# Performance work log

Measured on AMD Instinct MI355X. Metric: run time of the kernel, lower is better.

## Reference

```python
import jax, jax.numpy as jnp
import numpy as np

ALPHA, GAMMA, EPS = 0.25, 2.0, 1e-8
COST_CLASS, COST_BBOX, COST_GIOU = 2.0, 5.0, 2.0


def box_cxcywh_to_xyxy(b):
    cx, cy, w, h = jnp.split(b, 4, axis=-1)
    return jnp.concatenate([cx - 0.5 * w, cy - 0.5 * h, cx + 0.5 * w, cy + 0.5 * h], axis=-1)


def setup_inputs() -> dict:
    key = jax.random.key(0)
    k1, k2, k3, k4 = jax.random.split(key, 4)
    bs, Q, C, T = 16, 900, 80, 1600
    return {
        "pred_logits": jax.random.normal(k1, (bs, Q, C), jnp.float32),
        "pred_boxes": jax.random.uniform(k2, (bs, Q, 4), jnp.float32),
        "tgt_labels": jax.random.randint(k3, (T,), 0, C),
        "tgt_boxes": jax.random.uniform(k4, (T, 4), jnp.float32),
        "g_size": 3,
    }


def reference(pred_logits, pred_boxes, tgt_labels, tgt_boxes, g_size):
    bs, Q, _ = pred_logits.shape
    # focal classification cost (use_focal=True path)
    p = jax.nn.sigmoid(pred_logits.reshape(bs * Q, -1))  # [N, C]
    neg = (1.0 - ALPHA) * p ** GAMMA * (-jnp.log(1.0 - p + EPS))
    pos = ALPHA * (1.0 - p) ** GAMMA * (-jnp.log(p + EPS))
    cost_class = (pos - neg)[:, tgt_labels]  # [N, T]
    # L1 box cost (cdist p=1)
    out_bbox = pred_boxes.reshape(bs * Q, 4)
    cost_bbox = jnp.abs(out_bbox[:, None, :] - tgt_bbox_b(tgt_boxes)).sum(-1)  # [N, T]
    # GIoU cost
    b1 = box_cxcywh_to_xyxy(out_bbox)  # [N, 4]
    b2 = box_cxcywh_to_xyxy(tgt_boxes)  # [T, 4]
    area1 = (b1[:, 2] - b1[:, 0]) * (b1[:, 3] - b1[:, 1])
    area2 = (b2[:, 2] - b2[:, 0]) * (b2[:, 3] - b2[:, 1])
    lt = jnp.maximum(b1[:, None, :2], b2[None, :, :2])
    rb = jnp.minimum(b1[:, None, 2:], b2[None, :, 2:])
    wh = jnp.clip(rb - lt, 0.0)
    inter = wh[..., 0] * wh[..., 1]
    union = area1[:, None] + area2[None, :] - inter
    iou = inter / union
    elt = jnp.minimum(b1[:, None, :2], b2[None, :, :2])
    erb = jnp.maximum(b1[:, None, 2:], b2[None, :, 2:])
    ewh = jnp.clip(erb - elt, 0.0)
    earea = ewh[..., 0] * ewh[..., 1]
    giou = iou - (earea - union) / earea
    # weighted total cost, then group reduction (note: original names it Cmin but takes max over the group dim)
    Cmat = COST_BBOX * cost_bbox + COST_CLASS * cost_class + COST_GIOU * (-giou)
    Cmin = Cmat.reshape(bs, Q // g_size, g_size, -1).max(axis=2)  # [bs, Q//g, T]
    return Cmin


def tgt_bbox_b(tgt_boxes):
    return tgt_boxes[None, :, :]
```

## Files before the change

### kernel.cpp

```cpp
#include <hip/hip_runtime.h>

#define ALPHA 0.25f
#define EPS   1e-8f

constexpr int BS    = 16;
constexpr int QN    = 900;
constexpr int CN    = 80;
constexpr int GS    = 3;
constexpr int WAVES = 4;
constexpr int NT    = WAVES * 64;
constexpr int ROWS  = WAVES * GS;
constexpr int CCPAD = 16;

__global__ __launch_bounds__(NT) void fused_cost_kernel(
    const float* __restrict__ pred_logits,
    const float* __restrict__ pred_boxes,
    const int*   __restrict__ tgt_labels,
    const float* __restrict__ tgt_boxes,
    float*       __restrict__ out,
    int T)
{
    __shared__ __align__(16) float s_cc[CN * CCPAD];

    const int tid  = threadIdx.x;
    const int wv   = tid >> 6;
    const int lane = tid & 63;
    const int b    = blockIdx.y;
    const int n0   = b * QN + blockIdx.x * ROWS;

    const float* lg0 = pred_logits + (size_t)n0 * CN;
    for (int k = tid; k < ROWS * CN; k += NT) {
        const int r = k / CN, c = k - r * CN;
        float x = lg0[k];
        float p = __fdividef(1.0f, 1.0f + __expf(-x));
        float omp = 1.0f - p;
        float pos = ALPHA * omp * omp * (-__logf(p + EPS));
        float neg = (1.0f - ALPHA) * p * p * (-__logf(omp + EPS));
        s_cc[c * CCPAD + r + r / GS] = pos - neg;
    }

    float Pcx[GS], Pcy[GS], Pw[GS], Ph[GS];
    float Px0[GS], Py0[GS], Px1[GS], Py1[GS], Pa[GS];
    #pragma unroll
    for (int g = 0; g < GS; ++g) {
        const float4 pb = ((const float4*)pred_boxes)[n0 + wv * GS + g];
        Pcx[g] = pb.x;  Pcy[g] = pb.y;  Pw[g] = pb.z;  Ph[g] = pb.w;
        Px0[g] = pb.x - 0.5f * pb.z;  Py0[g] = pb.y - 0.5f * pb.w;
        Px1[g] = pb.x + 0.5f * pb.z;  Py1[g] = pb.y + 0.5f * pb.w;
        Pa[g]  = pb.z * pb.w;
    }
    __syncthreads();

    const int qg = blockIdx.x * WAVES + wv;
    float* __restrict__ outp = out + (size_t)(b * (QN / GS) + qg) * T;
    const int ccBase = wv * 4;

    for (int t = lane; t < T; t += 64) {
        const float4 tr = ((const float4*)tgt_boxes)[t];
        const int lab   = tgt_labels[t];
        const float tx0 = tr.x - 0.5f * tr.z, ty0 = tr.y - 0.5f * tr.w;
        const float tx1 = tr.x + 0.5f * tr.z, ty1 = tr.y + 0.5f * tr.w;
        const float ta  = tr.z * tr.w;

        const float4 cc4 = *(const float4*)&s_cc[lab * CCPAD + ccBase];
        const float ccv[GS] = { cc4.x, cc4.y, cc4.z };

        float m = -3.402823466e+38f;
        #pragma unroll
        for (int g = 0; g < GS; ++g) {
            float l1 = fabsf(Pcx[g] - tr.x) + fabsf(Pcy[g] - tr.y)
                     + fabsf(Pw[g]  - tr.z) + fabsf(Ph[g]  - tr.w);

            float iw = fminf(Px1[g], tx1) - fmaxf(Px0[g], tx0);
            float ih = fminf(Py1[g], ty1) - fmaxf(Py0[g], ty0);
            float inter = fmaxf(iw, 0.0f) * fmaxf(ih, 0.0f);
            float uni   = Pa[g] + ta - inter;

            float ew = fmaxf(Px1[g], tx1) - fminf(Px0[g], tx0);
            float eh = fmaxf(Py1[g], ty1) - fminf(Py0[g], ty0);
            float earea = ew * eh;

            float num = fmaf(inter, earea, uni * uni);
            float den = uni * earea;
            float g2  = 2.0f * __fdividef(num, den);

            float cost = fmaf(5.0f, l1, fmaf(2.0f, ccv[g], 2.0f - g2));
            m = fmaxf(m, cost);
        }
        outp[t] = m;
    }
}

extern "C" void kernel_launch(void* const* d_in, const int* in_sizes, int n_in,
                              void* d_out, int out_size, void* d_ws, size_t ws_size,
                              hipStream_t stream) {
    const float* pred_logits = (const float*)d_in[0];
    const float* pred_boxes  = (const float*)d_in[1];
    const int*   tgt_labels  = (const int*)d_in[2];
    const float* tgt_boxes   = (const float*)d_in[3];

    const int T = in_sizes[2];
    float* out = (float*)d_out;

    dim3 grid((QN / GS) / WAVES, BS);
    fused_cost_kernel<<<grid, NT, 0, stream>>>(
        pred_logits, pred_boxes, tgt_labels, tgt_boxes, out, T);
}
```

Before: 104.9 us.

## Split target dimension across blocks and simplify class-cost smem layout

Adds a grid dimension that splits the T targets into two halves per block, doubling the block count while each block recomputes the 12-row focal-cost table. The smem table becomes row-major with the constant offset and the factor of 2 folded in, replacing one float4 LDS with three scalar reads. The target loop is unrolled by two with an explicit tail. The cost is redundant sigmoid/log work, since each logit block is now computed twice. It also assumes T divides evenly by TSPLIT.

```diff
diff --git a/kernel.cpp b/kernel.cpp
--- a/kernel.cpp
+++ b/kernel.cpp
@@ -3,14 +3,14 @@
 #define ALPHA 0.25f
 #define EPS   1e-8f
 
-constexpr int BS    = 16;
-constexpr int QN    = 900;
-constexpr int CN    = 80;
-constexpr int GS    = 3;
-constexpr int WAVES = 4;
-constexpr int NT    = WAVES * 64;
-constexpr int ROWS  = WAVES * GS;
-constexpr int CCPAD = 16;
+constexpr int BS     = 16;
+constexpr int QN     = 900;
+constexpr int CN     = 80;
+constexpr int GS     = 3;
+constexpr int WAVES  = 4;
+constexpr int NT     = WAVES * 64;
+constexpr int ROWS   = WAVES * GS;
+constexpr int TSPLIT = 2;
 
 __global__ __launch_bounds__(NT) void fused_cost_kernel(
     const float* __restrict__ pred_logits,
@@ -20,23 +20,23 @@
     float*       __restrict__ out,
     int T)
 {
-    __shared__ __align__(16) float s_cc[CN * CCPAD];
+    __shared__ float s_cc[ROWS * CN];
 
     const int tid  = threadIdx.x;
     const int wv   = tid >> 6;
     const int lane = tid & 63;
-    const int b    = blockIdx.y;
-    const int n0   = b * QN + blockIdx.x * ROWS;
+    const int b    = blockIdx.z;
+    const int n0   = b * QN + blockIdx.y * ROWS;
 
     const float* lg0 = pred_logits + (size_t)n0 * CN;
+    #pragma unroll
     for (int k = tid; k < ROWS * CN; k += NT) {
-        const int r = k / CN, c = k - r * CN;
         float x = lg0[k];
         float p = __fdividef(1.0f, 1.0f + __expf(-x));
         float omp = 1.0f - p;
         float pos = ALPHA * omp * omp * (-__logf(p + EPS));
         float neg = (1.0f - ALPHA) * p * p * (-__logf(omp + EPS));
-        s_cc[c * CCPAD + r + r / GS] = pos - neg;
+        s_cc[k] = 2.0f * (pos - neg) + 2.0f;
     }
 
     float Pcx[GS], Pcy[GS], Pw[GS], Ph[GS];
@@ -51,19 +51,25 @@
     }
     __syncthreads();
 
-    const int qg = blockIdx.x * WAVES + wv;
+    const int qg = blockIdx.y * WAVES + wv;
     float* __restrict__ outp = out + (size_t)(b * (QN / GS) + qg) * T;
-    const int ccBase = wv * 4;
+    const int ccRow = (wv * GS) * CN;
 
-    for (int t = lane; t < T; t += 64) {
+    const int tChunk = T / TSPLIT;
+    const int t0     = blockIdx.x * tChunk;
+    const int nFull  = tChunk >> 6;
+    const int tail   = tChunk & 63;
+
+    auto body = [&](int t) {
         const float4 tr = ((const float4*)tgt_boxes)[t];
         const int lab   = tgt_labels[t];
         const float tx0 = tr.x - 0.5f * tr.z, ty0 = tr.y - 0.5f * tr.w;
         const float tx1 = tr.x + 0.5f * tr.z, ty1 = tr.y + 0.5f * tr.w;
         const float ta  = tr.z * tr.w;
 
-        const float4 cc4 = *(const float4*)&s_cc[lab * CCPAD + ccBase];
-        const float ccv[GS] = { cc4.x, cc4.y, cc4.z };
+        float ccs[GS];
+        #pragma unroll
+        for (int g = 0; g < GS; ++g) ccs[g] = s_cc[ccRow + g * CN + lab];
 
         float m = -3.402823466e+38f;
         #pragma unroll
@@ -81,14 +87,19 @@
             float earea = ew * eh;
 
             float num = fmaf(inter, earea, uni * uni);
-            float den = uni * earea;
-            float g2  = 2.0f * __fdividef(num, den);
+            float q   = __fdividef(num, uni * earea);
 
-            float cost = fmaf(5.0f, l1, fmaf(2.0f, ccv[g], 2.0f - g2));
+            float cost = fmaf(5.0f, l1, fmaf(-2.0f, q, ccs[g]));
             m = fmaxf(m, cost);
         }
         outp[t] = m;
-    }
+    };
+
+    #pragma unroll 2
+    for (int i = 0; i < nFull; ++i)
+        body(t0 + (i << 6) + lane);
+    if (lane < tail)
+        body(t0 + (nFull << 6) + lane);
 }
 
 extern "C" void kernel_launch(void* const* d_in, const int* in_sizes, int n_in,
@@ -102,7 +113,7 @@
     const int T = in_sizes[2];
     float* out = (float*)d_out;
 
-    dim3 grid((QN / GS) / WAVES, BS);
+    dim3 grid(TSPLIT, (QN / GS) / WAVES, BS);
     fused_cost_kernel<<<grid, NT, 0, stream>>>(
         pred_logits, pred_boxes, tgt_labels, tgt_boxes, out, T);
 }
```

After: 102.7 us. -2.1%, faster.

## Tile over targets and query groups with one target per thread

Applied to the files above, without the earlier changes.

The grid is restructured so each block covers 10 query groups and a 320-target tile, with each thread owning one target and looping over the groups. Before, each wave owned one group and looped over all targets. The class cost table is stored row-major with the 2x scale and +2 offset folded in. The enclosing-box area is derived from the intersection widths, which saves some min/max work. The goal is more parallelism, fewer redundant target loads per block and less arithmetic. The risks are that it assumes T is divisible by 320 with no bounds check, recomputes the focal cost for 30 rows per target tile, and reads pred boxes uniformly from global memory.

```diff
diff --git a/kernel.cpp b/kernel.cpp
--- a/kernel.cpp
+++ b/kernel.cpp
@@ -3,14 +3,15 @@
 #define ALPHA 0.25f
 #define EPS   1e-8f
 
-constexpr int BS    = 16;
-constexpr int QN    = 900;
-constexpr int CN    = 80;
-constexpr int GS    = 3;
-constexpr int WAVES = 4;
-constexpr int NT    = WAVES * 64;
-constexpr int ROWS  = WAVES * GS;
-constexpr int CCPAD = 16;
+constexpr int BS   = 16;
+constexpr int QN   = 900;
+constexpr int CN   = 80;
+constexpr int GS   = 3;
+constexpr int GPB  = 10;
+constexpr int ROWS = GPB * GS;
+constexpr int WAVES = 5;
+constexpr int NT   = WAVES * 64;
+constexpr int TPB  = NT;
 
 __global__ __launch_bounds__(NT) void fused_cost_kernel(
     const float* __restrict__ pred_logits,
@@ -20,74 +21,67 @@
     float*       __restrict__ out,
     int T)
 {
-    __shared__ __align__(16) float s_cc[CN * CCPAD];
+    __shared__ float s_cc[ROWS * CN];
 
-    const int tid  = threadIdx.x;
-    const int wv   = tid >> 6;
-    const int lane = tid & 63;
-    const int b    = blockIdx.y;
-    const int n0   = b * QN + blockIdx.x * ROWS;
+    const int tid = threadIdx.x;
+    const int b   = blockIdx.z;
+    const int qg0 = blockIdx.x * GPB;
+    const int n0  = b * QN + qg0 * GS;
 
     const float* lg0 = pred_logits + (size_t)n0 * CN;
     for (int k = tid; k < ROWS * CN; k += NT) {
-        const int r = k / CN, c = k - r * CN;
         float x = lg0[k];
         float p = __fdividef(1.0f, 1.0f + __expf(-x));
         float omp = 1.0f - p;
         float pos = ALPHA * omp * omp * (-__logf(p + EPS));
         float neg = (1.0f - ALPHA) * p * p * (-__logf(omp + EPS));
-        s_cc[c * CCPAD + r + r / GS] = pos - neg;
+        s_cc[k] = 2.0f * (pos - neg) + 2.0f;
     }
 
-    float Pcx[GS], Pcy[GS], Pw[GS], Ph[GS];
-    float Px0[GS], Py0[GS], Px1[GS], Py1[GS], Pa[GS];
-    #pragma unroll
-    for (int g = 0; g < GS; ++g) {
-        const float4 pb = ((const float4*)pred_boxes)[n0 + wv * GS + g];
-        Pcx[g] = pb.x;  Pcy[g] = pb.y;  Pw[g] = pb.z;  Ph[g] = pb.w;
-        Px0[g] = pb.x - 0.5f * pb.z;  Py0[g] = pb.y - 0.5f * pb.w;
-        Px1[g] = pb.x + 0.5f * pb.z;  Py1[g] = pb.y + 0.5f * pb.w;
-        Pa[g]  = pb.z * pb.w;
-    }
+    const int t  = blockIdx.y * TPB + tid;
+    const float4 tr = ((const float4*)tgt_boxes)[t];
+    const int   lab = tgt_labels[t];
+    const float tcx = tr.x, tcy = tr.y, tw = tr.z, th = tr.w;
+    const float tx0 = tcx - 0.5f * tw, ty0 = tcy - 0.5f * th;
+    const float tx1 = tcx + 0.5f * tw, ty1 = tcy + 0.5f * th;
+    const float ta  = tw * th;
+
     __syncthreads();
 
-    const int qg = blockIdx.x * WAVES + wv;
-    float* __restrict__ outp = out + (size_t)(b * (QN / GS) + qg) * T;
-    const int ccBase = wv * 4;
+    const float* ccLab = s_cc + lab;
+    float* __restrict__ outp = out + (size_t)(b * (QN / GS) + qg0) * T + t;
+    const float4* __restrict__ pb = (const float4*)pred_boxes + n0;
 
-    for (int t = lane; t < T; t += 64) {
-        const float4 tr = ((const float4*)tgt_boxes)[t];
-        const int lab   = tgt_labels[t];
-        const float tx0 = tr.x - 0.5f * tr.z, ty0 = tr.y - 0.5f * tr.w;
-        const float tx1 = tr.x + 0.5f * tr.z, ty1 = tr.y + 0.5f * tr.w;
-        const float ta  = tr.z * tr.w;
-
-        const float4 cc4 = *(const float4*)&s_cc[lab * CCPAD + ccBase];
-        const float ccv[GS] = { cc4.x, cc4.y, cc4.z };
-
+    #pragma unroll 2
+    for (int j = 0; j < GPB; ++j) {
         float m = -3.402823466e+38f;
         #pragma unroll
         for (int g = 0; g < GS; ++g) {
-            float l1 = fabsf(Pcx[g] - tr.x) + fabsf(Pcy[g] - tr.y)
-                     + fabsf(Pw[g]  - tr.z) + fabsf(Ph[g]  - tr.w);
+            const int r = j * GS + g;
+            const float4 pr = pb[r];
+            const float ccs = ccLab[r * CN];
 
-            float iw = fminf(Px1[g], tx1) - fmaxf(Px0[g], tx0);
-            float ih = fminf(Py1[g], ty1) - fmaxf(Py0[g], ty0);
+            const float px0 = pr.x - 0.5f * pr.z, py0 = pr.y - 0.5f * pr.w;
+            const float px1 = pr.x + 0.5f * pr.z, py1 = pr.y + 0.5f * pr.w;
+            const float pa  = pr.z * pr.w;
+
+            float l1 = fabsf(pr.x - tcx) + fabsf(pr.y - tcy)
+                     + fabsf(pr.z - tw)  + fabsf(pr.w - th);
+
+            float iw = fminf(px1, tx1) - fmaxf(px0, tx0);
+            float ih = fminf(py1, ty1) - fmaxf(py0, ty0);
             float inter = fmaxf(iw, 0.0f) * fmaxf(ih, 0.0f);
-            float uni   = Pa[g] + ta - inter;
+            float uni   = pa + ta - inter;
 
-            float ew = fmaxf(Px1[g], tx1) - fminf(Px0[g], tx0);
-            float eh = fmaxf(Py1[g], ty1) - fminf(Py0[g], ty0);
-            float earea = ew * eh;
+            float earea = (pr.z + tw - iw) * (pr.w + th - ih);
 
             float num = fmaf(inter, earea, uni * uni);
-            float den = uni * earea;
-            float g2  = 2.0f * __fdividef(num, den);
+            float q   = __fdividef(num, uni * earea);
 
-            float cost = fmaf(5.0f, l1, fmaf(2.0f, ccv[g], 2.0f - g2));
+            float cost = fmaf(5.0f, l1, fmaf(-2.0f, q, ccs));
             m = fmaxf(m, cost);
         }
-        outp[t] = m;
+        outp[(size_t)j * T] = m;
     }
 }
 
@@ -102,7 +96,7 @@
     const int T = in_sizes[2];
     float* out = (float*)d_out;
 
-    dim3 grid((QN / GS) / WAVES, BS);
+    dim3 grid((QN / GS) / GPB, T / TPB, BS);
     fused_cost_kernel<<<grid, NT, 0, stream>>>(
         pred_logits, pred_boxes, tgt_labels, tgt_boxes, out, T);
 }
```

Measured after the change: 112.0 us. +6.8%, slower.
